# Kernel tuning notes

Measured on AMD Instinct MI355X. Metric: run time of the kernel, lower is better.

The kernel has to match this reference:

```python
import jax, jax.numpy as jnp
import numpy as np
import math

B_SZ = 16384   # batch
IN_D = 1024    # input_dim
HD = 512       # hidden_dim
ID = 1024      # intermediate_dim = hidden_dim * expand_factor
S = 64         # state_dim
NL = 8         # num_layers
CD = 128       # condition_dim
DT_RANK = 1024 # must equal ID for source to broadcast


def setup_inputs() -> dict:
    key = jax.random.key(0)
    ks = iter(jax.random.split(key, 48))
    def nrm(shape, scale=0.02):
        return jax.random.normal(next(ks), shape, jnp.float32) * scale
    inp = {}
    inp["x"] = jax.random.normal(next(ks), (B_SZ, IN_D), jnp.float32)
    inp["timestep"] = jax.random.randint(next(ks), (B_SZ,), 0, 1000)
    inp["condition"] = jax.random.normal(next(ks), (B_SZ, CD), jnp.float32)
    inp["in_w"] = nrm((IN_D, HD)); inp["in_b"] = jnp.zeros((HD,))
    inp["t_w1"] = nrm((HD, 4 * HD)); inp["t_b1"] = jnp.zeros((4 * HD,))
    inp["t_w2"] = nrm((4 * HD, HD)); inp["t_b2"] = jnp.zeros((HD,))
    inp["c_w1"] = nrm((CD, HD)); inp["c_b1"] = jnp.zeros((HD,))
    inp["c_w2"] = nrm((HD, HD)); inp["c_b2"] = jnp.zeros((HD,))
    inp["norm_w"] = jnp.ones((NL, HD)); inp["norm_b"] = jnp.zeros((NL, HD))
    inp["inproj_w"] = nrm((NL, HD, 2 * ID)); inp["inproj_b"] = jnp.zeros((NL, 2 * ID))
    inp["conv_w"] = nrm((NL, ID, 1, 3), 0.3); inp["conv_b"] = jnp.zeros((NL, ID))
    inp["dt_w"] = nrm((NL, ID, DT_RANK)); inp["dt_b"] = jnp.zeros((NL, DT_RANK))
    inp["dt_bias"] = jax.random.uniform(next(ks), (NL, ID), jnp.float32)
    inp["A_log"] = jnp.tile(jnp.log(jnp.arange(1, S + 1, dtype=jnp.float32)), (NL, 1))
    inp["Dp"] = jnp.ones((NL, ID))
    inp["B_w"] = nrm((NL, ID, S)); inp["B_b"] = jnp.zeros((NL, S))
    inp["C_w"] = nrm((NL, ID, S)); inp["C_b"] = jnp.zeros((NL, S))
    inp["condp_w"] = nrm((NL, HD, ID)); inp["condp_b"] = jnp.zeros((NL, ID))
    inp["out_w"] = nrm((NL, ID, HD)); inp["out_b"] = jnp.zeros((NL, HD))
    inp["on_w"] = jnp.ones((HD,)); inp["on_b"] = jnp.zeros((HD,))
    inp["op_w"] = nrm((HD, IN_D)); inp["op_b"] = jnp.zeros((IN_D,))
    return inp


def _ln(x, w, b, eps=1e-5):
    m = jnp.mean(x, -1, keepdims=True)
    v = jnp.mean((x - m) ** 2, -1, keepdims=True)
    return (x - m) * jax.lax.rsqrt(v + eps) * w + b


def _selective_scan(x, dt_w, dt_b, dt_bias, A_log, Dp, B_w, B_b, C_w, C_b):
    # x: [B, L, ID]
    dt = jax.nn.softplus(x @ dt_w + dt_b + dt_bias)    # [B,L,DT_RANK]
    dt = jnp.mean(dt, -1, keepdims=True)               # [B,L,1]
    Bp = x @ B_w + B_b                                 # [B,L,S]
    Cp = x @ C_w + C_b                                 # [B,L,S]
    A = -jnp.exp(A_log)                                # [S]
    A_disc = jnp.exp(A * dt)                           # [B,L,S]
    Bx = (Bp * dt) * jnp.mean(x, -1, keepdims=True)    # [B,L,S]

    def step(h, inp):
        Ad_t, Bx_t, C_t = inp
        h = Ad_t * h + Bx_t
        return h, jnp.sum(C_t * h, -1)

    h0 = jnp.zeros((x.shape[0], A_log.shape[0]), x.dtype)
    _, ys = jax.lax.scan(
        step, h0,
        (jnp.swapaxes(A_disc, 0, 1), jnp.swapaxes(Bx, 0, 1), jnp.swapaxes(Cp, 0, 1)))
    y = jnp.swapaxes(ys, 0, 1)[..., None]              # [B,L,1] -> broadcast to [B,L,ID]
    return y + x * Dp


def reference(x, timestep, condition, in_w, in_b, t_w1, t_b1, t_w2, t_b2,
              c_w1, c_b1, c_w2, c_b2, norm_w, norm_b, inproj_w, inproj_b,
              conv_w, conv_b, dt_w, dt_b, dt_bias, A_log, Dp, B_w, B_b,
              C_w, C_b, condp_w, condp_b, out_w, out_b, on_w, on_b, op_w, op_b):
    h = x[:, None, :] @ in_w + in_b                    # [B,1,HD]
    half = HD // 2
    freqs = jnp.exp(-math.log(10000.0) * jnp.arange(half, dtype=jnp.float32) / half)
    args = timestep.astype(jnp.float32)[:, None] * freqs
    temb = jnp.concatenate([jnp.cos(args), jnp.sin(args)], -1)
    temb = jax.nn.silu(temb @ t_w1 + t_b1) @ t_w2 + t_b2
    cemb = jax.nn.silu(condition @ c_w1 + c_b1) @ c_w2 + c_b2
    cond = temb + cemb                                  # [B,HD]
    for i in range(NL):
        res = h
        hn = _ln(h, norm_w[i], norm_b[i])
        xp = hn @ inproj_w[i] + inproj_b[i]             # [B,1,2*ID]
        x_proj, gate = jnp.split(xp, 2, -1)
        xc = jnp.swapaxes(x_proj, 1, 2)                 # [B,ID,L]
        xc = jax.lax.conv_general_dilated(
            xc, conv_w[i], (1,), [(1, 1)],
            dimension_numbers=('NCH', 'OIH', 'NCH'), feature_group_count=ID)
        x_proj = jnp.swapaxes(xc + conv_b[i][None, :, None], 1, 2)
        x_proj = jax.nn.silu(x_proj)
        x_proj = x_proj + (cond @ condp_w[i] + condp_b[i])[:, None, :]
        y = _selective_scan(x_proj, dt_w[i], dt_b[i], dt_bias[i], A_log[i],
                            Dp[i], B_w[i], B_b[i], C_w[i], C_b[i])
        y = y * jax.nn.silu(gate)
        y = y @ out_w[i] + out_b[i]
        h = res + y
    h = _ln(h, on_w, on_b)
    out = h @ op_w + op_b
    return out[:, 0, :]
```

## Files before the change

### kernel.cpp

```cpp
#include <hip/hip_runtime.h>
#include <hip/hip_bf16.h>
#include <cstdint>
#include <cstddef>

typedef unsigned short u16;
typedef __attribute__((ext_vector_type(8))) short short8;
typedef __attribute__((ext_vector_type(4))) float float4v;

__device__ __forceinline__ float b2f(u16 u) {
  union { unsigned int i; float f; } v; v.i = ((unsigned int)u) << 16; return v.f;
}
__device__ __forceinline__ u16 f2b(float f) {
  union { float f; unsigned int i; } v; v.f = f;
  unsigned int r = v.i + 0x7fffu + ((v.i >> 16) & 1u);
  return (u16)(r >> 16);
}
__device__ __forceinline__ float silu_f(float v) { return v / (1.f + __expf(-v)); }
__device__ __forceinline__ float softplus_f(float v) {
  return fmaxf(v, 0.f) + __logf(1.f + __expf(-fabsf(v)));
}
__device__ __forceinline__ u16 ldx(const void* src, size_t i, int f32) {
  return f32 ? f2b(((const float*)src)[i]) : ((const u16*)src)[i];
}

#define GLD_LDS16(g, s) __builtin_amdgcn_global_load_lds( \
    (const __attribute__((address_space(1))) void*)(g),   \
    (__attribute__((address_space(3))) void*)(s), 16, 0, 0)

__global__ void probe_kernel(const void* w, int* flag)
{
  __shared__ int cnt;
  if (threadIdx.x == 0) cnt = 0;
  __syncthreads();
  const unsigned int* p = (const unsigned int*)w;
  int c = 0;
  for (int i = threadIdx.x; i < 1024; i += 256) {
    unsigned int lo = p[i] & 0xFFFFu;
    int e = (int)((lo >> 7) & 0xFFu);
    c += (e >= 100 && e <= 127) ? 1 : 0;
  }
  atomicAdd(&cnt, c);
  __syncthreads();
  if (threadIdx.x == 0) *flag = (cnt >= 512) ? 0 : 1;
}

struct SegTable { const void* src[20]; int off[20]; int cnt[20]; };
__global__ void convert_params(SegTable t, u16* dst, const int* flag)
{
  const int s = blockIdx.x;
  const int f32 = *flag;
  u16* d = dst + t.off[s];
  const int n = t.cnt[s];
  for (int i = threadIdx.x; i < n; i += 256) d[i] = ldx(t.src[s], i, f32);
}

__global__ void convert_off(const void* __restrict__ src, size_t eoff,
                            u16* __restrict__ dst, size_t n,
                            const int* __restrict__ flag)
{
  const size_t i = (size_t)blockIdx.x * 256 + threadIdx.x;
  if (i < n) dst[i] = ldx(src, eoff + i, *flag);
}

struct EpiP {
  const u16* bias;
  u16* outb;
  float* outf;
  const u16* add;
  const u16* cw;
  const u16* cb;
  const u16* cp;
  u16* xproj;
  u16* gate;
  const u16* dtb;
  const u16* dtbias;
  float* dtsum;
  float* bc;
  const int* dtf;
};

template<int EPI>
__global__ __launch_bounds__(256)
void gemm_bt(const u16* __restrict__ A, const u16* __restrict__ Bt,
             EpiP e, int M, int N, int K)
{
  __shared__ u16 As[128 * 32];
  __shared__ u16 Bs[128 * 32];
  const int tid  = threadIdx.x;
  const int lane = tid & 63;
  const int wave = tid >> 6;
  const int quad = lane >> 4;
  const int l15  = lane & 15;
  const int wr = (wave >> 1) << 6;
  const int wc = (wave & 1) << 6;
  const int bm = blockIdx.y * 128;
  const int bn = blockIdx.x * 128;

  const int r0 = tid >> 2;
  const int c0 = (tid & 3) << 3;
  const u16* Ab = A  + (size_t)(bm + r0) * K + c0;
  const u16* Bb = Bt + (size_t)(bn + r0) * K + c0;
  char* sA = (char*)As + tid * 16;
  char* sB = (char*)Bs + tid * 16;

  float4v acc[4][4] = {};

  for (int k0 = 0; k0 < K; k0 += 32) {
    GLD_LDS16(Ab + k0,                  sA);
    GLD_LDS16(Ab + (size_t)64 * K + k0, sA + 4096);
    GLD_LDS16(Bb + k0,                  sB);
    GLD_LDS16(Bb + (size_t)64 * K + k0, sB + 4096);
    __syncthreads();

    short8 aF[4], bF[4];
#pragma unroll
    for (int i = 0; i < 4; ++i) {
      aF[i] = *(const short8*)(As + (wr + i * 16 + l15) * 32 + quad * 8);
      bF[i] = *(const short8*)(Bs + (wc + i * 16 + l15) * 32 + quad * 8);
    }
#pragma unroll
    for (int mi = 0; mi < 4; ++mi)
#pragma unroll
      for (int ni = 0; ni < 4; ++ni)
        acc[mi][ni] = __builtin_amdgcn_mfma_f32_16x16x32_bf16(aF[mi], bF[ni], acc[mi][ni], 0, 0, 0);
    __syncthreads();
  }

  if (EPI == 6) {
    if (bn < 1024) {
#pragma unroll
      for (int mi = 0; mi < 4; ++mi) {
#pragma unroll
        for (int r = 0; r < 4; ++r) {
          float s = 0.f;
#pragma unroll
          for (int ni = 0; ni < 4; ++ni) {
            const int n = bn + wc + ni * 16 + l15;
            s += softplus_f(acc[mi][ni][r] + b2f(e.dtb[n]) + b2f(e.dtbias[n]));
          }
#pragma unroll
          for (int m = 1; m < 16; m <<= 1) s += __shfl_xor(s, m);
          if (l15 == 0)
            atomicAdd(&e.dtsum[bm + wr + mi * 16 + quad * 4 + r], s);
        }
      }
    } else {
#pragma unroll
      for (int mi = 0; mi < 4; ++mi)
#pragma unroll
        for (int ni = 0; ni < 4; ++ni) {
          const int row = bm + wr + mi * 16 + quad * 4;
          const int col = wc + ni * 16 + l15;
#pragma unroll
          for (int r = 0; r < 4; ++r)
            e.bc[(size_t)(row + r) * 128 + col] = acc[mi][ni][r];
        }
    }
    return;
  }

  float bv[4];
#pragma unroll
  for (int ni = 0; ni < 4; ++ni)
    bv[ni] = e.bias ? b2f(e.bias[bn + wc + ni * 16 + l15]) : 0.f;

  const int f32out = (EPI == 7) ? *e.dtf : 0;

#pragma unroll
  for (int mi = 0; mi < 4; ++mi) {
#pragma unroll
    for (int ni = 0; ni < 4; ++ni) {
      const int m = bm + wr + mi * 16 + quad * 4;
      const int n = bn + wc + ni * 16 + l15;
#pragma unroll
      for (int r = 0; r < 4; ++r) {
        float v = acc[mi][ni][r] + bv[ni];
        size_t idx = (size_t)(m + r) * N + n;
        if (EPI == 0)      e.outb[idx] = f2b(v);
        else if (EPI == 1) e.outb[idx] = f2b(silu_f(v));
        else if (EPI == 2) e.outf[idx] = e.outf[idx] + v;
        else if (EPI == 3) e.outb[idx] = f2b(v + b2f(e.add[idx]));
        else if (EPI == 5) e.outf[idx] = v;
        else if (EPI == 7) { if (f32out) e.outf[idx] = v; else e.outb[idx] = f2b(v); }
        else if (EPI == 4) {
          if (n < 1024) {
            float w = silu_f(v * b2f(e.cw[n * 3 + 1]) + b2f(e.cb[n]));
            size_t ix = (size_t)(m + r) * 1024 + n;
            e.xproj[ix] = f2b(w + b2f(e.cp[ix]));
          } else {
            e.gate[(size_t)(m + r) * 1024 + (n - 1024)] = f2b(v);
          }
        }
      }
    }
  }
}

__global__ __launch_bounds__(256)
void ln_kernel(const float* __restrict__ in, u16* __restrict__ out,
               const u16* __restrict__ w, const u16* __restrict__ b,
               float* __restrict__ dtsum)
{
  const int lane = threadIdx.x & 63;
  const int row  = blockIdx.x * 4 + (threadIdx.x >> 6);
  if (dtsum && lane == 0) dtsum[row] = 0.f;
  const float* x = in + (size_t)row * 512;
  float v[8], s = 0.f;
#pragma unroll
  for (int i = 0; i < 8; ++i) { v[i] = x[i * 64 + lane]; s += v[i]; }
#pragma unroll
  for (int m = 1; m < 64; m <<= 1) s += __shfl_xor(s, m);
  const float mean = s * (1.f / 512.f);
  float s2 = 0.f;
#pragma unroll
  for (int i = 0; i < 8; ++i) { float d = v[i] - mean; s2 += d * d; }
#pragma unroll
  for (int m = 1; m < 64; m <<= 1) s2 += __shfl_xor(s2, m);
  const float rs = rsqrtf(s2 * (1.f / 512.f) + 1e-5f);
  u16* o = out + (size_t)row * 512;
#pragma unroll
  for (int i = 0; i < 8; ++i) {
    int c = i * 64 + lane;
    o[c] = f2b((v[i] - mean) * rs * b2f(w[c]) + b2f(b[c]));
  }
}

__global__ void temb_kernel(const int* __restrict__ ts, u16* __restrict__ out)
{
  const int b = blockIdx.x, d = threadIdx.x;
  float t = (float)ts[b];
  float fr = __expf(-9.210340371976184f * (float)d * (1.f / 256.f));
  float a = t * fr;
  out[(size_t)b * 512 + d]       = f2b(cosf(a));
  out[(size_t)b * 512 + 256 + d] = f2b(sinf(a));
}

__global__ __launch_bounds__(256)
void scan_kernel(const float* __restrict__ bc, const float* __restrict__ dtsum,
                 const u16* __restrict__ xproj, const u16* __restrict__ gate,
                 const u16* __restrict__ B_b, const u16* __restrict__ C_b,
                 const u16* __restrict__ Dp, u16* __restrict__ y)
{
  const int lane = threadIdx.x & 63;
  const int row  = blockIdx.x * 4 + (threadIdx.x >> 6);
  const u16* xrow = xproj + (size_t)row * 1024;
  float xv[16], sx = 0.f;
#pragma unroll
  for (int i = 0; i < 16; ++i) { xv[i] = b2f(xrow[i * 64 + lane]); sx += xv[i]; }
  float bp  = bc[(size_t)row * 128 + lane]      + b2f(B_b[lane]);
  float cpv = bc[(size_t)row * 128 + 64 + lane] + b2f(C_b[lane]);
  float dot = bp * cpv;
#pragma unroll
  for (int m = 1; m < 64; m <<= 1) {
    sx  += __shfl_xor(sx, m);
    dot += __shfl_xor(dot, m);
  }
  const float scal = dot * (dtsum[row] * (1.f / 1024.f)) * (sx * (1.f / 1024.f));
  const u16* grow = gate + (size_t)row * 1024;
  u16* yrow = y + (size_t)row * 1024;
#pragma unroll
  for (int i = 0; i < 16; ++i) {
    int c = i * 64 + lane;
    yrow[c] = f2b((scal + xv[i] * b2f(Dp[c])) * silu_f(b2f(grow[c])));
  }
}

__global__ void transpose_kernel(const void* __restrict__ src, u16* __restrict__ dst,
                                 int K, int N, const int* flag)
{
  __shared__ u16 t[32][33];
  const int f32 = *flag;
  const int n0 = blockIdx.x * 32, k0 = blockIdx.y * 32;
  const int tx = threadIdx.x, ty = threadIdx.y;
#pragma unroll
  for (int i = 0; i < 32; i += 8)
    t[ty + i][tx] = ldx(src, (size_t)(k0 + ty + i) * N + n0 + tx, f32);
  __syncthreads();
#pragma unroll
  for (int i = 0; i < 32; i += 8)
    dst[(size_t)(n0 + ty + i) * K + k0 + tx] = t[tx][ty + i];
}

__global__ void transpose_layer(const void* __restrict__ ipw, const void* __restrict__ cpw,
                                const void* __restrict__ ow, const void* __restrict__ dtw,
                                const void* __restrict__ bw, const void* __restrict__ cw_,
                                int layer, u16* __restrict__ wbuf, const int* flag)
{
  __shared__ u16 t[32][33];
  const int f32 = *flag;
  int tb_ = blockIdx.x;
  const void* src; u16* dst; int K, N; size_t eoff;
  if (tb_ < 1024)      { src = ipw; dst = wbuf;           K = 512;  N = 2048; eoff = (size_t)layer * 512 * 2048; }
  else if (tb_ < 1536) { tb_ -= 1024; src = cpw; dst = wbuf + 1048576; K = 512;  N = 1024; eoff = (size_t)layer * 512 * 1024; }
  else if (tb_ < 2048) { tb_ -= 1536; src = ow;  dst = wbuf + 1572864; K = 1024; N = 512;  eoff = (size_t)layer * 1024 * 512; }
  else if (tb_ < 3072) { tb_ -= 2048; src = dtw; dst = wbuf + 2097152; K = 1024; N = 1024; eoff = (size_t)layer * 1024 * 1024; }
  else if (tb_ < 3136) { tb_ -= 3072; src = bw;  dst = wbuf + 2097152 + 1024 * 1024; K = 1024; N = 64; eoff = (size_t)layer * 1024 * 64; }
  else                 { tb_ -= 3136; src = cw_; dst = wbuf + 2097152 + 1088 * 1024; K = 1024; N = 64; eoff = (size_t)layer * 1024 * 64; }
  const int nt = tb_ % (N / 32), kt = tb_ / (N / 32);
  const int n0 = nt * 32, k0 = kt * 32;
  const int tx = threadIdx.x, ty = threadIdx.y;
#pragma unroll
  for (int i = 0; i < 32; i += 8)
    t[ty + i][tx] = ldx(src, eoff + (size_t)(k0 + ty + i) * N + n0 + tx, f32);
  __syncthreads();
#pragma unroll
  for (int i = 0; i < 32; i += 8)
    dst[(size_t)(n0 + ty + i) * K + k0 + tx] = t[tx][ty + i];
}

enum {
  P_in_b = 0, P_t_b1 = 512, P_t_b2 = 2560, P_c_b1 = 3072, P_c_b2 = 3584,
  P_op_b = 4096, P_on_w = 5120, P_on_b = 5632, P_norm_w = 6144,
  P_norm_b = 10240, P_inproj_b = 14336, P_condp_b = 30720, P_out_b = 38912,
  P_conv_w = 43008, P_conv_b = 67584, P_dt_b = 75776, P_dt_bias = 83968,
  P_B_b = 92160, P_C_b = 92672, P_Dp = 93184, P_TOTAL = 101376
};

extern "C" void kernel_launch(void* const* d_in, const int* in_sizes, int n_in,
                              void* d_out, int out_size, void* d_ws, size_t ws_size,
                              hipStream_t stream)
{
  const void* x        = d_in[0];
  const int*  tstep    = (const int*)d_in[1];
  const void* cond_in  = d_in[2];
  const void* in_w     = d_in[3];
  const void* in_b     = d_in[4];
  const void* t_w1     = d_in[5];
  const void* t_b1     = d_in[6];
  const void* t_w2     = d_in[7];
  const void* t_b2     = d_in[8];
  const void* c_w1     = d_in[9];
  const void* c_b1     = d_in[10];
  const void* c_w2     = d_in[11];
  const void* c_b2     = d_in[12];
  const void* norm_w   = d_in[13];
  const void* norm_b   = d_in[14];
  const void* inproj_w = d_in[15];
  const void* inproj_b = d_in[16];
  const void* conv_w   = d_in[17];
  const void* conv_b   = d_in[18];
  const void* dt_w     = d_in[19];
  const void* dt_b     = d_in[20];
  const void* dt_bias  = d_in[21];
  const void* Dp       = d_in[23];
  const void* B_w      = d_in[24];
  const void* B_b      = d_in[25];
  const void* C_w      = d_in[26];
  const void* C_b      = d_in[27];
  const void* condp_w  = d_in[28];
  const void* condp_b  = d_in[29];
  const void* out_w    = d_in[30];
  const void* out_b    = d_in[31];
  const void* on_w     = d_in[32];
  const void* on_b     = d_in[33];
  const void* op_w     = d_in[34];
  const void* op_b     = d_in[35];

  const int B = 16384;
  const size_t WB = (size_t)3276800 * 2;

  int c = 128;
  for (int cc = 1; cc <= 128; cc <<= 1) {
    size_t R = (size_t)B / cc;
    if (WB + 262144 + R * 13056 + 65536 <= ws_size) { c = cc; break; }
  }
  const int R = B / c;

  char* p = (char*)d_ws;
  auto alloc = [&](size_t bytes) {
    char* r = p; p += ((bytes + 255) & ~(size_t)255); return r;
  };
  int*   flag  = (int*)alloc(4);
  u16*   prm   = (u16*)alloc((size_t)P_TOTAL * 2);
  u16*   wbuf  = (u16*)alloc(WB);
  float* h     = (float*)alloc((size_t)R * 512 * 4);
  u16*   hn    = (u16*)alloc((size_t)R * 512 * 2);
  u16*   cond  = (u16*)alloc((size_t)R * 512 * 2);
  u16*   xg    = (u16*)alloc((size_t)R * 2048 * 2);
  u16*   cp    = (u16*)alloc((size_t)R * 1024 * 2);
  u16*   xbf   = (u16*)alloc((size_t)R * 1024 * 2);
  u16*   cbf   = (u16*)alloc((size_t)R * 128 * 2);
  float* bc    = (float*)alloc((size_t)R * 128 * 4);
  float* dtsum = (float*)alloc((size_t)R * 4);
  u16*   xproj = xg;
  u16*   gate  = xg + (size_t)R * 1024;

  probe_kernel<<<1, 256, 0, stream>>>(in_w, flag);
  {
    SegTable t;
    const void* s[20] = { in_b, t_b1, t_b2, c_b1, c_b2, op_b, on_w, on_b,
                          norm_w, norm_b, inproj_b, condp_b, out_b, conv_w,
                          conv_b, dt_b, dt_bias, B_b, C_b, Dp };
    const int o[20] = { P_in_b, P_t_b1, P_t_b2, P_c_b1, P_c_b2, P_op_b, P_on_w,
                        P_on_b, P_norm_w, P_norm_b, P_inproj_b, P_condp_b,
                        P_out_b, P_conv_w, P_conv_b, P_dt_b, P_dt_bias, P_B_b,
                        P_C_b, P_Dp };
    const int n[20] = { 512, 2048, 512, 512, 512, 1024, 512, 512, 4096, 4096,
                        16384, 8192, 4096, 24576, 8192, 8192, 8192, 512, 512,
                        8192 };
    for (int i = 0; i < 20; ++i) { t.src[i] = s[i]; t.off[i] = o[i]; t.cnt[i] = n[i]; }
    convert_params<<<20, 256, 0, stream>>>(t, prm, flag);
  }

  dim3 tblk(32, 8);
  auto T = [&](const void* s, u16* d, int K, int N) {
    transpose_kernel<<<dim3(N / 32, K / 32), tblk, 0, stream>>>(s, d, K, N, flag);
  };
  auto G = [&](int epi, const u16* A, const u16* Bt, EpiP e, int M, int N, int K) {
    dim3 g(N / 128, M / 128), blk(256);
    switch (epi) {
      case 0: gemm_bt<0><<<g, blk, 0, stream>>>(A, Bt, e, M, N, K); break;
      case 1: gemm_bt<1><<<g, blk, 0, stream>>>(A, Bt, e, M, N, K); break;
      case 2: gemm_bt<2><<<g, blk, 0, stream>>>(A, Bt, e, M, N, K); break;
      case 3: gemm_bt<3><<<g, blk, 0, stream>>>(A, Bt, e, M, N, K); break;
      case 4: gemm_bt<4><<<g, blk, 0, stream>>>(A, Bt, e, M, N, K); break;
      case 5: gemm_bt<5><<<g, blk, 0, stream>>>(A, Bt, e, M, N, K); break;
      case 6: gemm_bt<6><<<g, blk, 0, stream>>>(A, Bt, e, M, N, K); break;
      case 7: gemm_bt<7><<<g, blk, 0, stream>>>(A, Bt, e, M, N, K); break;
    }
  };

  for (int ci = 0; ci < c; ++ci) {
    const size_t row0 = (size_t)ci * R;
    const int* tsC = tstep + row0;
    u16*   outbC = (u16*)d_out + row0 * 1024;
    float* outfC = (float*)d_out + row0 * 1024;

    convert_off<<<(R * 1024) / 256, 256, 0, stream>>>(x, row0 * 1024, xbf,
                                                      (size_t)R * 1024, flag);
    convert_off<<<(R * 128) / 256, 256, 0, stream>>>(cond_in, row0 * 128, cbf,
                                                     (size_t)R * 128, flag);

    EpiP e0 = {};

    temb_kernel<<<R, 256, 0, stream>>>(tsC, hn);
    T(t_w1, wbuf, 512, 2048);
    { EpiP e = e0; e.bias = prm + P_t_b1; e.outb = xg;
      G(1, hn, wbuf, e, R, 2048, 512); }
    T(t_w2, wbuf, 2048, 512);
    { EpiP e = e0; e.bias = prm + P_t_b2; e.outb = cond;
      G(0, xg, wbuf, e, R, 512, 2048); }
    T(c_w1, wbuf, 128, 512);
    { EpiP e = e0; e.bias = prm + P_c_b1; e.outb = hn;
      G(1, cbf, wbuf, e, R, 512, 128); }
    T(c_w2, wbuf, 512, 512);
    { EpiP e = e0; e.bias = prm + P_c_b2; e.outb = cond; e.add = cond;
      G(3, hn, wbuf, e, R, 512, 512); }
    T(in_w, wbuf, 1024, 512);
    { EpiP e = e0; e.bias = prm + P_in_b; e.outf = h;
      G(5, xbf, wbuf, e, R, 512, 1024); }

    for (int i = 0; i < 8; ++i) {
      transpose_layer<<<3200, tblk, 0, stream>>>(
          inproj_w, condp_w, out_w, dt_w, B_w, C_w, i, wbuf, flag);
      ln_kernel<<<R / 4, 256, 0, stream>>>(h, hn, prm + P_norm_w + i * 512,
                                           prm + P_norm_b + i * 512, dtsum);
      { EpiP e = e0; e.bias = prm + P_condp_b + i * 1024; e.outb = cp;
        G(0, cond, wbuf + 1048576, e, R, 1024, 512); }
      { EpiP e = e0; e.bias = prm + P_inproj_b + i * 2048;
        e.cw = prm + P_conv_w + i * 3072; e.cb = prm + P_conv_b + i * 1024;
        e.cp = cp; e.xproj = xproj; e.gate = gate;
        G(4, hn, wbuf, e, R, 2048, 512); }
      { EpiP e = e0; e.dtb = prm + P_dt_b + i * 1024;
        e.dtbias = prm + P_dt_bias + i * 1024; e.dtsum = dtsum; e.bc = bc;
        G(6, xproj, wbuf + 2097152, e, R, 1152, 1024); }
      scan_kernel<<<R / 4, 256, 0, stream>>>(
          bc, dtsum, xproj, gate, prm + P_B_b + i * 64, prm + P_C_b + i * 64,
          prm + P_Dp + i * 1024, cp );
      { EpiP e = e0; e.bias = prm + P_out_b + i * 512; e.outf = h;
        G(2, cp, wbuf + 1572864, e, R, 512, 1024); }
    }

    ln_kernel<<<R / 4, 256, 0, stream>>>(h, hn, prm + P_on_w, prm + P_on_b,
                                         nullptr);
    T(op_w, wbuf, 512, 1024);
    { EpiP e = e0; e.bias = prm + P_op_b; e.outb = outbC; e.outf = outfC;
      e.dtf = flag;
      G(7, hn, wbuf, e, R, 1024, 512); }
  }
}
```

Baseline: 3.087 ms.

## Stage GEMM epilogue through LDS for vectorized stores and remap blocks per XCD

Bf16-output GEMM epilogues (plain, silu, residual-add, in-proj split) now write accumulators into a per-wave LDS staging tile and read them back row-contiguous, so each lane issues one 16-byte store instead of many scattered 2-byte stores. The grid becomes 1D and block indices are remapped so that blocks landing on the same XCD (round-robin by flat id) cover a contiguous band of M rows, which improves L2 reuse of the A tiles. Shared memory grows to hold the padded staging buffer, and the remap applies only when the M block count is a multiple of 8.

```diff
diff --git a/kernel.cpp b/kernel.cpp
--- a/kernel.cpp
+++ b/kernel.cpp
@@ -84,8 +84,9 @@
 void gemm_bt(const u16* __restrict__ A, const u16* __restrict__ Bt,
              EpiP e, int M, int N, int K)
 {
-  __shared__ u16 As[128 * 32];
-  __shared__ u16 Bs[128 * 32];
+  __shared__ u16 S[8704];
+  u16* As = S;
+  u16* Bs = S + 4096;
   const int tid  = threadIdx.x;
   const int lane = tid & 63;
   const int wave = tid >> 6;
@@ -93,8 +94,21 @@
   const int l15  = lane & 15;
   const int wr = (wave >> 1) << 6;
   const int wc = (wave & 1) << 6;
-  const int bm = blockIdx.y * 128;
-  const int bn = blockIdx.x * 128;
+
+  const int NBN = N >> 7, NBM = M >> 7;
+  int bm, bn;
+  {
+    const int flat = blockIdx.x;
+    if ((NBM & 7) == 0) {
+      const int xcd = flat & 7;
+      const int s = flat >> 3;
+      bn = (s % NBN) << 7;
+      bm = (xcd * (NBM >> 3) + s / NBN) << 7;
+    } else {
+      bn = (flat % NBN) << 7;
+      bm = (flat / NBN) << 7;
+    }
+  }
 
   const int r0 = tid >> 2;
   const int c0 = (tid & 3) << 3;
@@ -164,8 +178,65 @@
   for (int ni = 0; ni < 4; ++ni)
     bv[ni] = e.bias ? b2f(e.bias[bn + wc + ni * 16 + l15]) : 0.f;
 
+  if (EPI == 0 || EPI == 1 || EPI == 3 || EPI == 4) {
+    float* stg = (float*)S + wave * 1088;
+    const int rrow = lane >> 3;
+    const int ccol = (lane & 7) << 3;
+#pragma unroll
+    for (int mi = 0; mi < 4; ++mi) {
+#pragma unroll
+      for (int ni = 0; ni < 4; ++ni)
+#pragma unroll
+        for (int r = 0; r < 4; ++r)
+          stg[(quad * 4 + r) * 68 + ni * 16 + l15] = acc[mi][ni][r] + bv[ni];
+#pragma unroll
+      for (int half = 0; half < 2; ++half) {
+        const int lrow = rrow + half * 8;
+        const int gm = bm + wr + mi * 16 + lrow;
+        const int gn = bn + wc + ccol;
+        float vv[8];
+#pragma unroll
+        for (int j = 0; j < 8; ++j) vv[j] = stg[lrow * 68 + ccol + j];
+        u16 ov[8];
+        u16* dst;
+        if (EPI == 0) {
+#pragma unroll
+          for (int j = 0; j < 8; ++j) ov[j] = f2b(vv[j]);
+          dst = e.outb + (size_t)gm * N + gn;
+        } else if (EPI == 1) {
+#pragma unroll
+          for (int j = 0; j < 8; ++j) ov[j] = f2b(silu_f(vv[j]));
+          dst = e.outb + (size_t)gm * N + gn;
+        } else if (EPI == 3) {
+          const u16* ar = e.add + (size_t)gm * N + gn;
+#pragma unroll
+          for (int j = 0; j < 8; ++j) ov[j] = f2b(vv[j] + b2f(ar[j]));
+          dst = e.outb + (size_t)gm * N + gn;
+        } else {
+          if (gn < 1024) {
+            const size_t ix = (size_t)gm * 1024 + gn;
+            const u16* cr = e.cp + ix;
+#pragma unroll
+            for (int j = 0; j < 8; ++j) {
+              float w = silu_f(vv[j] * b2f(e.cw[(gn + j) * 3 + 1]) +
+                               b2f(e.cb[gn + j]));
+              ov[j] = f2b(w + b2f(cr[j]));
+            }
+            dst = e.xproj + ix;
+          } else {
+            const size_t ix = (size_t)gm * 1024 + (gn - 1024);
+#pragma unroll
+            for (int j = 0; j < 8; ++j) ov[j] = f2b(vv[j]);
+            dst = e.gate + ix;
+          }
+        }
+        *(short8*)dst = *(const short8*)ov;
+      }
+    }
+    return;
+  }
+
   const int f32out = (EPI == 7) ? *e.dtf : 0;
-
 #pragma unroll
   for (int mi = 0; mi < 4; ++mi) {
 #pragma unroll
@@ -176,21 +247,9 @@
       for (int r = 0; r < 4; ++r) {
         float v = acc[mi][ni][r] + bv[ni];
         size_t idx = (size_t)(m + r) * N + n;
-        if (EPI == 0)      e.outb[idx] = f2b(v);
-        else if (EPI == 1) e.outb[idx] = f2b(silu_f(v));
-        else if (EPI == 2) e.outf[idx] = e.outf[idx] + v;
-        else if (EPI == 3) e.outb[idx] = f2b(v + b2f(e.add[idx]));
+        if (EPI == 2)      e.outf[idx] = e.outf[idx] + v;
         else if (EPI == 5) e.outf[idx] = v;
         else if (EPI == 7) { if (f32out) e.outf[idx] = v; else e.outb[idx] = f2b(v); }
-        else if (EPI == 4) {
-          if (n < 1024) {
-            float w = silu_f(v * b2f(e.cw[n * 3 + 1]) + b2f(e.cb[n]));
-            size_t ix = (size_t)(m + r) * 1024 + n;
-            e.xproj[ix] = f2b(w + b2f(e.cp[ix]));
-          } else {
-            e.gate[(size_t)(m + r) * 1024 + (n - 1024)] = f2b(v);
-          }
-        }
       }
     }
   }
@@ -407,7 +466,7 @@
     transpose_kernel<<<dim3(N / 32, K / 32), tblk, 0, stream>>>(s, d, K, N, flag);
   };
   auto G = [&](int epi, const u16* A, const u16* Bt, EpiP e, int M, int N, int K) {
-    dim3 g(N / 128, M / 128), blk(256);
+    dim3 g((N / 128) * (M / 128)), blk(256);
     switch (epi) {
       case 0: gemm_bt<0><<<g, blk, 0, stream>>>(A, Bt, e, M, N, K); break;
       case 1: gemm_bt<1><<<g, blk, 0, stream>>>(A, Bt, e, M, N, K); break;
```

Measured after the change: 2.805 ms. 9.1% less time.
